# Kernel tuning notes

Measured on AMD Instinct MI355X. Metric: run time of the kernel, lower is better.

Reference implementation:

```python
import jax, jax.numpy as jnp
import numpy as np

B, T, D = 4, 4096, 1024
P = 64  # d_model / n_head

def setup_inputs() -> dict:
    key = jax.random.key(0)
    k1, k2, k3 = jax.random.split(key, 3)
    x = jax.random.normal(k1, (B, T, D), dtype=jnp.float32)
    Wqkv = jax.random.normal(k2, (D, 3 * P), dtype=jnp.float32) * (1.0 / np.sqrt(D))
    bqkv = jax.random.normal(k3, (3 * P,), dtype=jnp.float32) * 0.01
    return {"x": x, "Wqkv": Wqkv, "bqkv": bqkv}

def reference(x, Wqkv, bqkv):
    Bv, Tv, Cv = x.shape
    qkv = (x @ Wqkv + bqkv).reshape(Bv, Tv, 3, P)  # [B,T,3,p]
    q, k, v = qkv[:, :, 0, :], qkv[:, :, 1, :], qkv[:, :, 2, :]
    # raw scores (source applies NO 1/sqrt(p) scaling)
    S = jnp.einsum('btp,bsp->bts', q, k)  # [B,T,T]
    causal = jnp.tril(jnp.ones((Tv, Tv), dtype=bool))
    S = jnp.where(causal[None, :, :], S, jnp.float32(-jnp.inf))
    Pm = jax.nn.softmax(S, axis=-1)
    O = jnp.einsum('bts,bsp->btp', Pm, v)  # [B,T,p]
    return O
```

## Files before the change

kernel.cpp:

```cpp
#include <hip/hip_runtime.h>
#include <hip/hip_fp16.h>

#define B_ 4
#define T_ 4096
#define D_ 1024

typedef _Float16 h8 __attribute__((ext_vector_type(8)));
typedef _Float16 h4 __attribute__((ext_vector_type(4)));
typedef float f32x4 __attribute__((ext_vector_type(4)));

#define LOG2E 1.44269504088896340736f
#define MASKV -3.0e38f
#define MINIT -1.0e30f
#define EXP2(x) __builtin_amdgcn_exp2f(x)

__global__ __launch_bounds__(256) void wt_kernel(const float* __restrict__ W,
                                                 _Float16* __restrict__ Wt) {
    __shared__ _Float16 Tr[192][20];
    const int tid = threadIdx.x, k0 = blockIdx.x * 16;
#pragma unroll
    for (int i = 0; i < 3; i++) {
        int fi = tid + 256 * i;
        int r = fi / 48, c4 = fi % 48;
        float4 v = *(const float4*)(W + (size_t)(k0 + r) * 192 + c4 * 4);
        Tr[c4 * 4 + 0][r] = (_Float16)v.x;
        Tr[c4 * 4 + 1][r] = (_Float16)v.y;
        Tr[c4 * 4 + 2][r] = (_Float16)v.z;
        Tr[c4 * 4 + 3][r] = (_Float16)v.w;
    }
    __syncthreads();
#pragma unroll
    for (int i = 0; i < 3; i++) {
        int oi = tid + 256 * i;
        int n = oi >> 2, kq = oi & 3;
        *(h4*)(Wt + (size_t)n * D_ + k0 + kq * 4) = *(const h4*)&Tr[n][kq * 4];
    }
}

__global__ __launch_bounds__(256) void proj_kernel(
    const float* __restrict__ x, const _Float16* __restrict__ Wt,
    const float* __restrict__ bias,
    _Float16* __restrict__ qh, _Float16* __restrict__ kh, _Float16* __restrict__ vh)
{
    __shared__ __align__(16) char psm[35840];
    _Float16* Asp = (_Float16*)psm;
    _Float16* Bsp = (_Float16*)(psm + 5120);
    _Float16* Ostp = (_Float16*)psm;
    const int tid = threadIdx.x;
    const int w = tid >> 6, lane = tid & 63, quad = lane >> 4, l16 = lane & 15;
    const int row0 = blockIdx.x * 32;
    const int mstrip = w & 1;
    const int ngrp = (w >> 1) * 6;

    float bvals[6];
#pragma unroll
    for (int nt = 0; nt < 6; nt++) bvals[nt] = bias[(ngrp + nt) * 16 + l16];

    f32x4 acc[6];
#pragma unroll
    for (int i = 0; i < 6; i++) acc[i] = (f32x4){0.f, 0.f, 0.f, 0.f};

    const int arow = tid >> 3, ac0 = (tid & 7) * 4;

    float4 xa;
    h8 wreg[3];
    {
        xa = *(const float4*)(x + (size_t)(row0 + arow) * D_ + ac0);
#pragma unroll
        for (int p = 0; p < 3; p++) {
            int f = tid + 256 * p; int n = f >> 2, c0 = (f & 3) * 8;
            wreg[p] = *(const h8*)(Wt + (size_t)n * D_ + c0);
        }
    }

    for (int kc = 0; kc < 32; kc++) {
        const int buf = kc & 1;
        h4 av;
        av[0]=(_Float16)xa.x; av[1]=(_Float16)xa.y; av[2]=(_Float16)xa.z; av[3]=(_Float16)xa.w;
        *(h4*)(Asp + buf * 1280 + arow * 40 + ac0) = av;
#pragma unroll
        for (int p = 0; p < 3; p++) {
            int f = tid + 256 * p; int n = f >> 2, c0 = (f & 3) * 8;
            *(h8*)(Bsp + buf * 7680 + n * 40 + c0) = wreg[p];
        }
        __syncthreads();
        if (kc + 1 < 32) {
            int k0 = (kc + 1) * 32;
            xa = *(const float4*)(x + (size_t)(row0 + arow) * D_ + k0 + ac0);
#pragma unroll
            for (int p = 0; p < 3; p++) {
                int f = tid + 256 * p; int n = f >> 2, c0 = (f & 3) * 8;
                wreg[p] = *(const h8*)(Wt + (size_t)n * D_ + k0 + c0);
            }
        }
        h8 a0 = *(const h8*)(Asp + buf * 1280 + (16 * mstrip + l16) * 40 + quad * 8);
#pragma unroll
        for (int nt = 0; nt < 6; nt++) {
            h8 b0 = *(const h8*)(Bsp + buf * 7680 + ((ngrp + nt) * 16 + l16) * 40 + quad * 8);
            acc[nt] = __builtin_amdgcn_mfma_f32_16x16x32_f16(a0, b0, acc[nt], 0, 0, 0);
        }
    }

    __syncthreads();
#pragma unroll
    for (int nt = 0; nt < 6; nt++) {
        int n = (ngrp + nt) * 16 + l16;
        float scale = (n < 64) ? LOG2E : 1.0f;
#pragma unroll
        for (int reg = 0; reg < 4; reg++)
            Ostp[(16 * mstrip + quad * 4 + reg) * 200 + n] =
                (_Float16)((acc[nt][reg] + bvals[nt]) * scale);
    }
    __syncthreads();
    {
        const int mrow = tid >> 3, c0 = (tid & 7) * 8;
        _Float16* dsts[3] = {qh, kh, vh};
#pragma unroll
        for (int g = 0; g < 3; g++)
            *(h8*)(dsts[g] + (size_t)(row0 + mrow) * 64 + c0) =
                *(const h8*)(Ostp + mrow * 200 + g * 64 + c0);
    }
}

__global__ __launch_bounds__(256, 2) void attn_kernel(
    const _Float16* __restrict__ qh, const _Float16* __restrict__ kh,
    const _Float16* __restrict__ vh, float* __restrict__ out,
    _Float16* __restrict__ Opart, float2* __restrict__ ml,
    int lgC, int NC1, int direct, int q8, int total)
{
    __shared__ _Float16 Ks[2][64][72];
    __shared__ _Float16 Vt[2][64][72];
    const int tid = threadIdx.x;
    const int w = tid >> 6, lane = tid & 63, quad = lane >> 4, l16 = lane & 15;
    const int C = 1 << lgC;

    const int bid = blockIdx.x;
    const int cid = (bid & 7) * q8 + (bid >> 3);
    if (cid >= total) return;

    const int b = cid / NC1;
    int rem = cid - b * NC1;
    int qt2 = 0, k0 = 0, cnt = 1;
    for (int i = 0; i < 32; i++) {
        int nc = (2 * i + 2 + C - 1) >> lgC;
        if (rem < nc) { qt2 = i; k0 = rem << lgC; cnt = min(C, 2 * i + 2 - k0); break; }
        rem -= nc;
    }
    const size_t base = (size_t)b * T_ * 64;
    const int qbase = qt2 * 128 + w * 32;

    h8 qf[2][2];
#pragma unroll
    for (int u = 0; u < 2; u++) {
        const _Float16* qp = qh + base + (size_t)(qbase + u * 16 + l16) * 64 + quad * 8;
        qf[u][0] = *(const h8*)qp;
        qf[u][1] = *(const h8*)(qp + 32);
    }

    f32x4 o[8];
#pragma unroll
    for (int i = 0; i < 8; i++) o[i] = (f32x4){0.f, 0.f, 0.f, 0.f};
    float m[2] = {MINIT, MINIT}, l[2] = {0.f, 0.f};

    const int krow = tid >> 3, kc0 = (tid & 7) * 8;
    const int vp0 = (tid & 15) * 4, vc0 = (tid >> 4) * 4;
    h8 kreg[2];
    h4 vreg[4];
    {
        const _Float16* kp = kh + base + (size_t)(k0 * 64) * 64;
        kreg[0] = *(const h8*)(kp + (size_t)krow * 64 + kc0);
        kreg[1] = *(const h8*)(kp + (size_t)(krow + 32) * 64 + kc0);
        const _Float16* vp = vh + base + (size_t)(k0 * 64 + vc0) * 64 + vp0;
#pragma unroll
        for (int i = 0; i < 4; i++) vreg[i] = *(const h4*)(vp + (size_t)i * 64);
    }

    const int kend = k0 + cnt;
    for (int kt = k0; kt < kend; kt++) {
        const int buf = kt & 1;
        *(h8*)&Ks[buf][krow][kc0] = kreg[0];
        *(h8*)&Ks[buf][krow + 32][kc0] = kreg[1];
#pragma unroll
        for (int j = 0; j < 4; j++) {
            h4 t;
            t[0] = vreg[0][j]; t[1] = vreg[1][j]; t[2] = vreg[2][j]; t[3] = vreg[3][j];
            *(h4*)&Vt[buf][vp0 + j][vc0] = t;
        }
        __syncthreads();
        if (kt + 1 < kend) {
            const _Float16* kp = kh + base + (size_t)((kt + 1) * 64) * 64;
            kreg[0] = *(const h8*)(kp + (size_t)krow * 64 + kc0);
            kreg[1] = *(const h8*)(kp + (size_t)(krow + 32) * 64 + kc0);
            const _Float16* vp = vh + base + (size_t)((kt + 1) * 64 + vc0) * 64 + vp0;
#pragma unroll
            for (int i = 0; i < 4; i++) vreg[i] = *(const h4*)(vp + (size_t)i * 64);
        }

        const bool skip = (kt * 64) > (qbase + 31);
        if (!skip) {
            f32x4 s[2][4];
#pragma unroll
            for (int nt = 0; nt < 4; nt++) {
                h8 kf0 = *(const h8*)&Ks[buf][nt * 16 + l16][quad * 8];
                h8 kf1 = *(const h8*)&Ks[buf][nt * 16 + l16][32 + quad * 8];
#pragma unroll
                for (int u = 0; u < 2; u++) {
                    f32x4 c = (f32x4){0.f, 0.f, 0.f, 0.f};
                    c = __builtin_amdgcn_mfma_f32_16x16x32_f16(kf0, qf[u][0], c, 0, 0, 0);
                    c = __builtin_amdgcn_mfma_f32_16x16x32_f16(kf1, qf[u][1], c, 0, 0, 0);
                    s[u][nt] = c;
                }
            }

            h4 pf[2][4];
#pragma unroll
            for (int u = 0; u < 2; u++) {
                const int qrow = qbase + u * 16 + l16;
                if (kt * 64 + 63 > qbase + u * 16) {
#pragma unroll
                    for (int nt = 0; nt < 4; nt++)
#pragma unroll
                        for (int reg = 0; reg < 4; reg++) {
                            int sg = kt * 64 + nt * 16 + quad * 4 + reg;
                            if (sg > qrow) s[u][nt][reg] = MASKV;
                        }
                }
                float mx = s[u][0][0];
#pragma unroll
                for (int nt = 0; nt < 4; nt++)
#pragma unroll
                    for (int reg = 0; reg < 4; reg++) mx = fmaxf(mx, s[u][nt][reg]);
                mx = fmaxf(mx, __shfl_xor(mx, 16));
                mx = fmaxf(mx, __shfl_xor(mx, 32));
                float mnew = fmaxf(m[u], mx);
                float alpha = EXP2(m[u] - mnew);
                m[u] = mnew;
                float rs = 0.f;
#pragma unroll
                for (int nt = 0; nt < 4; nt++) {
                    h4 ph;
#pragma unroll
                    for (int reg = 0; reg < 4; reg++) {
                        float p = EXP2(s[u][nt][reg] - mnew);
                        rs += p;
                        ph[reg] = (_Float16)p;
                    }
                    pf[u][nt] = ph;
                }
                rs += __shfl_xor(rs, 16);
                rs += __shfl_xor(rs, 32);
                l[u] = l[u] * alpha + rs;
#pragma unroll
                for (int pt = 0; pt < 4; pt++)
#pragma unroll
                    for (int reg = 0; reg < 4; reg++) o[u * 4 + pt][reg] *= alpha;
            }

#pragma unroll
            for (int pt = 0; pt < 4; pt++)
#pragma unroll
                for (int nt = 0; nt < 4; nt++) {
                    h4 vf = *(const h4*)&Vt[buf][pt * 16 + l16][nt * 16 + quad * 4];
                    o[pt]     = __builtin_amdgcn_mfma_f32_16x16x16f16(vf, pf[0][nt], o[pt], 0, 0, 0);
                    o[4 + pt] = __builtin_amdgcn_mfma_f32_16x16x16f16(vf, pf[1][nt], o[4 + pt], 0, 0, 0);
                }
        }
    }

    if (direct) {
#pragma unroll
        for (int u = 0; u < 2; u++) {
            float linv = 1.0f / l[u];
            int trow = qt2 * 128 + w * 32 + u * 16 + l16;
#pragma unroll
            for (int pt = 0; pt < 4; pt++)
#pragma unroll
                for (int reg = 0; reg < 4; reg++)
                    out[base + (size_t)trow * 64 + pt * 16 + quad * 4 + reg] =
                        o[u * 4 + pt][reg] * linv;
        }
    } else {
        __syncthreads();
        _Float16* St = &Ks[0][0][0];
#pragma unroll
        for (int u = 0; u < 2; u++) {
            int r = w * 32 + u * 16 + l16;
#pragma unroll
            for (int pt = 0; pt < 4; pt++) {
                h4 ph;
#pragma unroll
                for (int reg = 0; reg < 4; reg++) ph[reg] = (_Float16)o[u * 4 + pt][reg];
                *(h4*)&St[r * 72 + pt * 16 + quad * 4] = ph;
            }
            if (quad == 0) ml[(size_t)cid * 128 + r] = make_float2(m[u], l[u]);
        }
        __syncthreads();
        _Float16* op = Opart + (size_t)cid * 8192;
        const int r = tid >> 1, c0 = (tid & 1) * 32;
#pragma unroll
        for (int j = 0; j < 4; j++)
            *(h8*)(op + r * 64 + c0 + 8 * j) = *(const h8*)&St[r * 72 + c0 + 8 * j];
    }
}

__global__ __launch_bounds__(256) void combine_kernel(
    const _Float16* __restrict__ Opart, const float2* __restrict__ ml,
    float* __restrict__ out, int lgC, int NC1)
{
    const int C = 1 << lgC;
    const int task = blockIdx.x;
    const int b = task >> 8, tile = (task >> 3) & 31, rg = task & 7;
    int pref = 0;
    for (int i = 0; i < tile; i++) pref += (2 * i + 2 + C - 1) >> lgC;
    const int cbase = b * NC1 + pref;
    const int nch = (2 * tile + 2 + C - 1) >> lgC;

    const int r = rg * 16 + (threadIdx.x >> 4);
    const int c0 = (threadIdx.x & 15) * 4;

    float M = MINIT;
    for (int i = 0; i < nch; i++) M = fmaxf(M, ml[(size_t)(cbase + i) * 128 + r].x);
    float L = 0.f, acc[4] = {0.f, 0.f, 0.f, 0.f};
    for (int i = 0; i < nch; i++) {
        float2 v = ml[(size_t)(cbase + i) * 128 + r];
        float sc = EXP2(v.x - M);
        L += sc * v.y;
        h4 x4 = *(const h4*)(Opart + (size_t)(cbase + i) * 8192 + (size_t)r * 64 + c0);
#pragma unroll
        for (int t = 0; t < 4; t++) acc[t] += sc * (float)x4[t];
    }
    float inv = 1.0f / L;
    float4 res = { acc[0]*inv, acc[1]*inv, acc[2]*inv, acc[3]*inv };
    *(float4*)(out + ((size_t)b * T_ + tile * 128 + r) * 64 + c0) = res;
}

extern "C" void kernel_launch(void* const* d_in, const int* in_sizes, int n_in,
                              void* d_out, int out_size, void* d_ws, size_t ws_size,
                              hipStream_t stream) {
    const float* x    = (const float*)d_in[0];
    const float* W    = (const float*)d_in[1];
    const float* bias = (const float*)d_in[2];
    float* out = (float*)d_out;
    char* ws = (char*)d_ws;
    _Float16* qh = (_Float16*)(ws);
    _Float16* kh = (_Float16*)(ws + (size_t)2 * 1024 * 1024);
    _Float16* vh = (_Float16*)(ws + (size_t)4 * 1024 * 1024);
    _Float16* Wt = (_Float16*)(ws + (size_t)6 * 1024 * 1024);
    const size_t pbase = (size_t)8 * 1024 * 1024;

    int lgC = -1, nc1 = 32;
    for (int lg = 2; lg <= 6; lg++) {
        int C = 1 << lg, n1 = 0;
        for (int i = 0; i < 32; i++) n1 += (2 * i + 2 + C - 1) >> lg;
        size_t need = pbase + (size_t)4 * n1 * (8192 * 2 + 128 * 8);
        if (need <= ws_size) { lgC = lg; nc1 = n1; break; }
    }
    int direct = (lgC < 0) ? 1 : 0;
    if (direct) { lgC = 6; nc1 = 32; }
    _Float16* Opart = (_Float16*)(ws + pbase);
    float2*   mlp   = (float2*)(ws + pbase + (size_t)4 * nc1 * 8192 * 2);

    const int total = 4 * nc1;
    const int q8 = (total + 7) / 8;

    wt_kernel<<<64, 256, 0, stream>>>(W, Wt);
    proj_kernel<<<512, 256, 0, stream>>>(x, Wt, bias, qh, kh, vh);
    attn_kernel<<<8 * q8, 256, 0, stream>>>(qh, kh, vh, out, Opart, mlp,
                                            lgC, nc1, direct, q8, total);
    if (!direct)
        combine_kernel<<<1024, 256, 0, stream>>>(Opart, mlp, out, lgC, nc1);
}
```

Before: 161.3 us.

## Widen projection K-chunk to 128 with single-buffered LDS; move attention barrier after prefetch

The QKV projection kernel now stages 128-wide K chunks (8 iterations instead of 32) in a single LDS buffer, with more registers per thread holding prefetched x and W. Each chunk runs four MFMA k-steps per barrier, so there are fewer barriers and larger, more coalesced global loads. The cost is more LDS (about 60KB) and higher register pressure, which could reduce occupancy. In the attention kernel the barrier moves after the next-tile global prefetch is issued, so the loads go out before the wait.

```diff
diff --git a/kernel.cpp b/kernel.cpp
--- a/kernel.cpp
+++ b/kernel.cpp
@@ -37,14 +37,14 @@
     }
 }
 
-__global__ __launch_bounds__(256) void proj_kernel(
+__global__ __launch_bounds__(256, 2) void proj_kernel(
     const float* __restrict__ x, const _Float16* __restrict__ Wt,
     const float* __restrict__ bias,
     _Float16* __restrict__ qh, _Float16* __restrict__ kh, _Float16* __restrict__ vh)
 {
-    __shared__ __align__(16) char psm[35840];
+    __shared__ __align__(16) char psm[60928];
     _Float16* Asp = (_Float16*)psm;
-    _Float16* Bsp = (_Float16*)(psm + 5120);
+    _Float16* Bsp = (_Float16*)(psm + 8704);
     _Float16* Ostp = (_Float16*)psm;
     const int tid = threadIdx.x;
     const int w = tid >> 6, lane = tid & 63, quad = lane >> 4, l16 = lane & 15;
@@ -60,44 +60,52 @@
 #pragma unroll
     for (int i = 0; i < 6; i++) acc[i] = (f32x4){0.f, 0.f, 0.f, 0.f};
 
-    const int arow = tid >> 3, ac0 = (tid & 7) * 4;
-
-    float4 xa;
-    h8 wreg[3];
-    {
-        xa = *(const float4*)(x + (size_t)(row0 + arow) * D_ + ac0);
-#pragma unroll
-        for (int p = 0; p < 3; p++) {
-            int f = tid + 256 * p; int n = f >> 2, c0 = (f & 3) * 8;
-            wreg[p] = *(const h8*)(Wt + (size_t)n * D_ + c0);
-        }
-    }
-
-    for (int kc = 0; kc < 32; kc++) {
-        const int buf = kc & 1;
-        h4 av;
-        av[0]=(_Float16)xa.x; av[1]=(_Float16)xa.y; av[2]=(_Float16)xa.z; av[3]=(_Float16)xa.w;
-        *(h4*)(Asp + buf * 1280 + arow * 40 + ac0) = av;
-#pragma unroll
-        for (int p = 0; p < 3; p++) {
-            int f = tid + 256 * p; int n = f >> 2, c0 = (f & 3) * 8;
-            *(h8*)(Bsp + buf * 7680 + n * 40 + c0) = wreg[p];
+    const int arow = tid >> 3, ac = (tid & 7) * 4;
+    const float* xrow = x + (size_t)(row0 + arow) * D_;
+
+    float4 xa[4];
+    h8 wreg[12];
+#pragma unroll
+    for (int p = 0; p < 4; p++) xa[p] = *(const float4*)(xrow + p * 32 + ac);
+#pragma unroll
+    for (int p = 0; p < 12; p++) {
+        int f = tid + 256 * p; int n = f >> 4, c = (f & 15) * 8;
+        wreg[p] = *(const h8*)(Wt + (size_t)n * D_ + c);
+    }
+
+    for (int it = 0; it < 8; it++) {
+        if (it) __syncthreads();
+#pragma unroll
+        for (int p = 0; p < 4; p++) {
+            h4 av;
+            av[0] = (_Float16)xa[p].x; av[1] = (_Float16)xa[p].y;
+            av[2] = (_Float16)xa[p].z; av[3] = (_Float16)xa[p].w;
+            *(h4*)(Asp + arow * 136 + p * 32 + ac) = av;
+        }
+#pragma unroll
+        for (int p = 0; p < 12; p++) {
+            int f = tid + 256 * p; int n = f >> 4, c = (f & 15) * 8;
+            *(h8*)(Bsp + n * 136 + c) = wreg[p];
         }
         __syncthreads();
-        if (kc + 1 < 32) {
-            int k0 = (kc + 1) * 32;
-            xa = *(const float4*)(x + (size_t)(row0 + arow) * D_ + k0 + ac0);
-#pragma unroll
-            for (int p = 0; p < 3; p++) {
-                int f = tid + 256 * p; int n = f >> 2, c0 = (f & 3) * 8;
-                wreg[p] = *(const h8*)(Wt + (size_t)n * D_ + k0 + c0);
-            }
-        }
-        h8 a0 = *(const h8*)(Asp + buf * 1280 + (16 * mstrip + l16) * 40 + quad * 8);
-#pragma unroll
-        for (int nt = 0; nt < 6; nt++) {
-            h8 b0 = *(const h8*)(Bsp + buf * 7680 + ((ngrp + nt) * 16 + l16) * 40 + quad * 8);
-            acc[nt] = __builtin_amdgcn_mfma_f32_16x16x32_f16(a0, b0, acc[nt], 0, 0, 0);
+        if (it + 1 < 8) {
+            const int k0 = (it + 1) * 128;
+#pragma unroll
+            for (int p = 0; p < 4; p++) xa[p] = *(const float4*)(xrow + k0 + p * 32 + ac);
+#pragma unroll
+            for (int p = 0; p < 12; p++) {
+                int f = tid + 256 * p; int n = f >> 4, c = (f & 15) * 8;
+                wreg[p] = *(const h8*)(Wt + (size_t)n * D_ + k0 + c);
+            }
+        }
+#pragma unroll
+        for (int kk = 0; kk < 4; kk++) {
+            h8 a0 = *(const h8*)(Asp + (16 * mstrip + l16) * 136 + kk * 32 + quad * 8);
+#pragma unroll
+            for (int nt = 0; nt < 6; nt++) {
+                h8 b0 = *(const h8*)(Bsp + ((ngrp + nt) * 16 + l16) * 136 + kk * 32 + quad * 8);
+                acc[nt] = __builtin_amdgcn_mfma_f32_16x16x32_f16(a0, b0, acc[nt], 0, 0, 0);
+            }
         }
     }
 
@@ -186,7 +194,6 @@
             t[0] = vreg[0][j]; t[1] = vreg[1][j]; t[2] = vreg[2][j]; t[3] = vreg[3][j];
             *(h4*)&Vt[buf][vp0 + j][vc0] = t;
         }
-        __syncthreads();
         if (kt + 1 < kend) {
             const _Float16* kp = kh + base + (size_t)((kt + 1) * 64) * 64;
             kreg[0] = *(const h8*)(kp + (size_t)krow * 64 + kc0);
@@ -195,6 +202,7 @@
 #pragma unroll
             for (int i = 0; i < 4; i++) vreg[i] = *(const h4*)(vp + (size_t)i * 64);
         }
+        __syncthreads();
 
         const bool skip = (kt * 64) > (qbase + 31);
         if (!skip) {
```

New measurement: 146.3 us. 1.1x faster.
